# Kernel optimization log

Hardware: AMD Instinct MI355X
Metric: run time of the kernel (lower is better)

## Reference

```python
import jax, jax.numpy as jnp
import numpy as np

B, S, D, H = 2, 2048, 64, 12  # batch, seq, richness (per-head dim), heads
NEG = -99999.0


def setup_inputs() -> dict:
    key = jax.random.key(0)
    ks = jax.random.split(key, 9)
    s_in = 1.0 / np.sqrt(D)
    s_out = 1.0 / np.sqrt(H * D)
    return {
        "x": jax.random.normal(ks[0], (B, S, D), dtype=jnp.float32),
        "Wq": jax.random.uniform(ks[1], (D, H * D), jnp.float32, -s_in, s_in),
        "bq": jax.random.uniform(ks[2], (H * D,), jnp.float32, -s_in, s_in),
        "Wk": jax.random.uniform(ks[3], (D, H * D), jnp.float32, -s_in, s_in),
        "bk": jax.random.uniform(ks[4], (H * D,), jnp.float32, -s_in, s_in),
        "Wv": jax.random.uniform(ks[5], (D, H * D), jnp.float32, -s_in, s_in),
        "bv": jax.random.uniform(ks[6], (H * D,), jnp.float32, -s_in, s_in),
        "Wo": jax.random.uniform(ks[7], (H * D, D), jnp.float32, -s_out, s_out),
        "bo": jax.random.uniform(ks[8], (D,), jnp.float32, -s_out, s_out),
    }


def reference(x, Wq, bq, Wk, bk, Wv, bv, Wo, bo):
    b, s, d = x.shape
    def split_heads(y):
        return y.reshape(b, s, H, d).transpose(0, 2, 1, 3)  # [B,H,S,D]
    q = split_heads(x @ Wq + bq)
    k = split_heads(x @ Wk + bk)
    v = split_heads(x @ Wv + bv)
    # NOTE: no 1/sqrt(d) scaling, faithful to original module.
    scores = jnp.einsum("bhqd,bhkd->bhqk", q, k)  # [B,H,S,S]
    # Faithful quirky mask: tril of the scores, then mask where it's zero.
    mask = jnp.tril(scores)
    scores = jnp.where(mask == 0, NEG, scores)
    p = jax.nn.softmax(scores, axis=-1)
    o = jnp.einsum("bhqk,bhkd->bhqd", p, v)  # [B,H,S,D]
    o = o.transpose(0, 2, 1, 3).reshape(b, s, H * d)
    return o @ Wo + bo
```

## Files before the change

### kernel.cpp

```cpp
#include <hip/hip_runtime.h>
#include <math.h>
#include <type_traits>

#define BB 2
#define SS 2048
#define DD 64
#define HH 12
#define C2FIX 23.083120654223414f

typedef _Float16 v8h __attribute__((ext_vector_type(8)));
typedef short    v8s __attribute__((ext_vector_type(8)));
typedef short    v4s __attribute__((ext_vector_type(4)));
typedef float    v4f __attribute__((ext_vector_type(4)));
typedef unsigned int v2u __attribute__((ext_vector_type(2)));

__device__ __forceinline__ unsigned short f2bf(float f) {
    unsigned u = __float_as_uint(f);
    u += 0x7FFF + ((u >> 16) & 1);
    return (unsigned short)(u >> 16);
}

__device__ __forceinline__ void async16(const void* g, void* l) {
    __builtin_amdgcn_global_load_lds(
        (const __attribute__((address_space(1))) unsigned int*)g,
        (__attribute__((address_space(3))) unsigned int*)l, 16, 0, 0);
}

__global__ __launch_bounds__(256) void prep_kernel(
    const float* __restrict__ x,
    const float* __restrict__ Wq, const float* __restrict__ Wk,
    const float* __restrict__ Wv, const float* __restrict__ Wo,
    _Float16* __restrict__ x16, _Float16* __restrict__ W16,
    _Float16* __restrict__ WoT)
{
    const int idx = blockIdx.x * 256 + threadIdx.x;
    if (idx < 262144) {
        x16[idx] = (_Float16)x[idx];
    } else if (idx < 262144 + 147456) {
        const int t = idx - 262144;
        const int k = t / 2304, c = t % 2304;
        const int mat = c / 768, cc = c % 768;
        const float* W = (mat == 0) ? Wq : (mat == 1) ? Wk : Wv;
        W16[c * 64 + k] = (_Float16)W[k * 768 + cc];
    } else {
        const int e = idx - 262144 - 147456;
        WoT[(e & 63) * 768 + (e >> 6)] = (_Float16)Wo[e];
    }
}

__global__ __launch_bounds__(256) void qkv_kernel(
    const _Float16* __restrict__ x16, const _Float16* __restrict__ W16,
    const float* __restrict__ bq, const float* __restrict__ bk,
    const float* __restrict__ bv,
    _Float16* __restrict__ Q16, _Float16* __restrict__ K16,
    unsigned short* __restrict__ VT)
{
    const int r0  = blockIdx.x * 64;
    const int c0g = blockIdx.y * 64;
    const int mat = c0g / 768, cc0 = c0g % 768;
    const int h   = cc0 >> 6;
    const int b   = r0 >> 11, s0 = r0 & 2047;

    const int wave = threadIdx.x >> 6, lane = threadIdx.x & 63;
    const int llow = lane & 15, quad = lane >> 4;
    const int rowbase = r0 + 16 * wave;

    const float* bias = (mat == 0) ? bq : (mat == 1) ? bk : bv;

    v8h a0 = *(const v8h*)(x16 + (size_t)(rowbase + llow) * 64 + quad * 8);
    v8h a1 = *(const v8h*)(x16 + (size_t)(rowbase + llow) * 64 + 32 + quad * 8);

    v4f acc[4];
    float bv4[4];
#pragma unroll
    for (int nb = 0; nb < 4; nb++) {
        const int col = c0g + 16 * nb + llow;
        v8h b0 = *(const v8h*)(W16 + (size_t)col * 64 + quad * 8);
        v8h b1 = *(const v8h*)(W16 + (size_t)col * 64 + 32 + quad * 8);
        v4f a = (v4f){0.f, 0.f, 0.f, 0.f};
        a = __builtin_amdgcn_mfma_f32_16x16x32_f16(a0, b0, a, 0, 0, 0);
        a = __builtin_amdgcn_mfma_f32_16x16x32_f16(a1, b1, a, 0, 0, 0);
        acc[nb] = a;
        bv4[nb] = bias[cc0 + 16 * nb + llow];
    }

    const int bh = b * HH + h;
    if (mat == 0) {
#pragma unroll
        for (int nb = 0; nb < 4; nb++)
#pragma unroll
            for (int r = 0; r < 4; r++) {
                const int s = s0 + 16 * wave + quad * 4 + r;
                Q16[((size_t)bh * SS + s) * 64 + 16 * nb + llow] =
                    (_Float16)((acc[nb][r] + bv4[nb]) * 1.4426950408889634f);
            }
    } else if (mat == 1) {
#pragma unroll
        for (int nb = 0; nb < 4; nb++)
#pragma unroll
            for (int r = 0; r < 4; r++) {
                const int s = s0 + 16 * wave + quad * 4 + r;
                K16[((size_t)bh * SS + s) * 64 + 16 * nb + llow] =
                    (_Float16)(acc[nb][r] + bv4[nb]);
            }
    } else {
#pragma unroll
        for (int nb = 0; nb < 4; nb++) {
            const int d = 16 * nb + llow;
            const int s = s0 + 16 * wave + quad * 4;
            unsigned short p0 = f2bf(acc[nb][0] + bv4[nb]);
            unsigned short p1 = f2bf(acc[nb][1] + bv4[nb]);
            unsigned short p2 = f2bf(acc[nb][2] + bv4[nb]);
            unsigned short p3 = f2bf(acc[nb][3] + bv4[nb]);
            v2u pk = (v2u){(unsigned)p0 | ((unsigned)p1 << 16),
                           (unsigned)p2 | ((unsigned)p3 << 16)};
            *(v2u*)&VT[((size_t)bh * 64 + d) * SS + s] = pk;
        }
    }
}

__global__ __launch_bounds__(256, 4) void attn_kernel(
    const _Float16* __restrict__ Q16, const _Float16* __restrict__ K16,
    const unsigned short* __restrict__ VTg, _Float16* __restrict__ O16)
{
    __shared__ __align__(16) _Float16       Kl[2][64 * 64];
    __shared__ __align__(16) unsigned short Vl[2][64 * 64];

    const int bh    = blockIdx.y;
    const int qtile = (int)((blockIdx.x + 11 * blockIdx.y) & 31);
    const int qBase = qtile * 64;
    const int wave  = threadIdx.x >> 6;
    const int lane  = threadIdx.x & 63;
    const int llow  = lane & 15;
    const int quad  = lane >> 4;
    const int q0    = qBase + 16 * wave;

    const _Float16*       Kp = K16 + (size_t)bh * SS * 64;
    const unsigned short* Vp = VTg + (size_t)bh * 64 * SS;

    const _Float16* Qp = Q16 + ((size_t)bh * SS + q0) * 64;
    v8h qa0 = *(const v8h*)(Qp + llow * 64 + quad * 8);
    v8h qa1 = *(const v8h*)(Qp + llow * 64 + 32 + quad * 8);

    v4f o[4];
    v4f ls = (v4f){0.f, 0.f, 0.f, 0.f};
    const short one_bf = (short)0x3F80;
    const v4s vones = (v4s){one_bf, one_bf, one_bf, one_bf};
#pragma unroll
    for (int nb = 0; nb < 4; nb++) o[nb] = (v4f){0.f, 0.f, 0.f, 0.f};

    const int nt = qtile + 1;
    const int qrow = q0 + llow;
    const int sw = llow & 7;

#pragma unroll
    for (int rep = 0; rep < 2; rep++) {
        int c = rep * 256 + threadIdx.x;
        int row = c >> 3, g = (c & 7) ^ (row & 7);
        async16(Kp + (size_t)row * 64 + g * 8, &Kl[0][(rep * 256 + wave * 64) * 8]);
        async16(Vp + (size_t)row * SS + g * 8, &Vl[0][(rep * 256 + wave * 64) * 8]);
    }

    auto tile_body = [&](int t, auto masked_c) {
        constexpr bool MASKED = decltype(masked_c)::value;
        __syncthreads();
        if (t + 1 < nt) {
            const int ktn = (t + 1) * 64, bufn = (t + 1) & 1;
#pragma unroll
            for (int rep = 0; rep < 2; rep++) {
                int c = rep * 256 + threadIdx.x;
                int row = c >> 3, g = (c & 7) ^ (row & 7);
                async16(Kp + (size_t)(ktn + row) * 64 + g * 8,
                        &Kl[bufn][(rep * 256 + wave * 64) * 8]);
                async16(Vp + (size_t)row * SS + ktn + g * 8,
                        &Vl[bufn][(rep * 256 + wave * 64) * 8]);
            }
        }
        const int buf = t & 1, kt = t * 64;

        v4f sc[4];
#pragma unroll
        for (int cb = 0; cb < 4; cb++) {
            const int rk = 16 * cb + llow;
            v8h k0 = *(const v8h*)&Kl[buf][rk * 64 + ((quad ^ sw)) * 8];
            v8h k1 = *(const v8h*)&Kl[buf][rk * 64 + (((4 + quad) ^ sw)) * 8];
            v4f a2 = (v4f){0.f, 0.f, 0.f, 0.f};
            a2 = __builtin_amdgcn_mfma_f32_16x16x32_f16(k0, qa0, a2, 0, 0, 0);
            a2 = __builtin_amdgcn_mfma_f32_16x16x32_f16(k1, qa1, a2, 0, 0, 0);
            sc[cb] = a2;
        }

        v4s vvf[4][4];
#pragma unroll
        for (int nb = 0; nb < 4; nb++) {
            const int rv = 16 * nb + llow;
#pragma unroll
            for (int cb = 0; cb < 4; cb++)
                vvf[nb][cb] = *(const v4s*)&Vl[buf][rv * 64 +
                                (((2 * cb + (quad >> 1)) ^ sw) * 8) + (quad & 1) * 4];
        }

        v4s pA[4];
#pragma unroll
        for (int cb = 0; cb < 4; cb++) {
            const int kbase = kt + 16 * cb + quad * 4;
            unsigned dw[2];
#pragma unroll
            for (int h2 = 0; h2 < 2; h2++) {
                float pv2[2];
#pragma unroll
                for (int j2 = 0; j2 < 2; j2++) {
                    const int r = h2 * 2 + j2;
                    const float sv = sc[cb][r];
                    const float e  = __builtin_amdgcn_exp2f(sv - C2FIX);
                    float p;
                    if constexpr (MASKED)
                        p = (kbase + r <= qrow && sv != 0.f) ? e : 0.f;
                    else
                        p = (sv != 0.f) ? e : 0.f;
                    pv2[j2] = p;
                }
                dw[h2] = __builtin_amdgcn_perm(__float_as_uint(pv2[1]),
                                               __float_as_uint(pv2[0]),
                                               0x07060302u);
            }
            v2u pk = (v2u){dw[0], dw[1]};
            pA[cb] = *(const v4s*)&pk;
        }

#pragma unroll
        for (int cb = 0; cb < 4; cb++)
            ls = __builtin_amdgcn_mfma_f32_16x16x16bf16_1k(pA[cb], vones, ls, 0, 0, 0);

#pragma unroll
        for (int nb = 0; nb < 4; nb++)
#pragma unroll
            for (int cb = 0; cb < 4; cb++)
                o[nb] = __builtin_amdgcn_mfma_f32_16x16x16bf16_1k(
                            pA[cb], vvf[nb][cb], o[nb], 0, 0, 0);
    };

    for (int t = 0; t < nt - 1; t++) tile_body(t, std::false_type{});
    tile_body(nt - 1, std::true_type{});

    float ir[4];
#pragma unroll
    for (int r = 0; r < 4; r++)
        ir[r] = 1.0f / ls[r];
    _Float16* Op = O16 + ((size_t)bh * SS + q0) * 64;
#pragma unroll
    for (int nb = 0; nb < 4; nb++)
#pragma unroll
        for (int r = 0; r < 4; r++)
            Op[(quad * 4 + r) * 64 + 16 * nb + llow] = (_Float16)(o[nb][r] * ir[r]);
}

__global__ __launch_bounds__(256) void out_kernel(
    const _Float16* __restrict__ O16, const _Float16* __restrict__ WoT,
    const float* __restrict__ bo, float* __restrict__ out)
{
    __shared__ __align__(16) float red[4][16][66];
    const int r0   = blockIdx.x * 16;
    const int wave = threadIdx.x >> 6, lane = threadIdx.x & 63;
    const int llow = lane & 15, quad = lane >> 4;
    const int b = r0 >> 11, s = r0 & 2047;

    v4f acc[4];
#pragma unroll
    for (int cb = 0; cb < 4; cb++) acc[cb] = (v4f){0.f, 0.f, 0.f, 0.f};

#pragma unroll
    for (int i = 0; i < 6; i++) {
        const int kb = wave * 6 + i;
        const int h = kb >> 1, dseg = (kb & 1) * 32;
        v8h af = *(const v8h*)(O16 + ((size_t)(b * HH + h) * SS + s + llow) * 64 + dseg + quad * 8);
#pragma unroll
        for (int cb = 0; cb < 4; cb++) {
            v8h bf = *(const v8h*)(WoT + (size_t)(16 * cb + llow) * 768 + kb * 32 + quad * 8);
            acc[cb] = __builtin_amdgcn_mfma_f32_16x16x32_f16(af, bf, acc[cb], 0, 0, 0);
        }
    }

#pragma unroll
    for (int cb = 0; cb < 4; cb++)
#pragma unroll
        for (int r = 0; r < 4; r++)
            red[wave][quad * 4 + r][16 * cb + llow] = acc[cb][r];
    __syncthreads();

    const int col = threadIdx.x & 63, rr = threadIdx.x >> 6;
    const float bias = bo[col];
    for (int i = rr; i < 16; i += 4) {
        float sum = red[0][i][col] + red[1][i][col] + red[2][i][col] + red[3][i][col] + bias;
        out[(size_t)(r0 + i) * 64 + col] = sum;
    }
}

extern "C" void kernel_launch(void* const* d_in, const int* in_sizes, int n_in,
                              void* d_out, int out_size, void* d_ws, size_t ws_size,
                              hipStream_t stream)
{
    const float* x  = (const float*)d_in[0];
    const float* Wq = (const float*)d_in[1];
    const float* bq = (const float*)d_in[2];
    const float* Wk = (const float*)d_in[3];
    const float* bk = (const float*)d_in[4];
    const float* Wv = (const float*)d_in[5];
    const float* bv = (const float*)d_in[6];
    const float* Wo = (const float*)d_in[7];
    const float* bo = (const float*)d_in[8];
    float* out = (float*)d_out;

    char* w = (char*)d_ws;
    const size_t MB = 1024 * 1024;
    _Float16*       x16 = (_Float16*)(w);
    _Float16*       W16 = (_Float16*)(w + 512 * 1024);
    _Float16*       WoT = (_Float16*)(w + 832 * 1024);
    _Float16*       Q16 = (_Float16*)(w + 1 * MB);
    _Float16*       K16 = (_Float16*)(w + 7 * MB);
    unsigned short* VT  = (unsigned short*)(w + 13 * MB);
    _Float16*       O16 = (_Float16*)(w + 19 * MB);

    prep_kernel<<<1792, 256, 0, stream>>>(x, Wq, Wk, Wv, Wo, x16, W16, WoT);
    qkv_kernel<<<dim3(64, 36), 256, 0, stream>>>(x16, W16, bq, bk, bv, Q16, K16, VT);
    attn_kernel<<<dim3(32, BB * HH), 256, 0, stream>>>(Q16, K16, VT, O16);
    out_kernel<<<(BB * SS) / 16, 256, 0, stream>>>(O16, WoT, bo, out);
}
```

Baseline: 135.7 us.

## Triple-buffer K/V tiles with explicit vmcnt waits for deeper prefetch

```diff
diff --git a/kernel.cpp b/kernel.cpp
--- a/kernel.cpp
+++ b/kernel.cpp
@@ -119,12 +119,12 @@
     }
 }
 
-__global__ __launch_bounds__(256, 4) void attn_kernel(
+__global__ __launch_bounds__(256, 3) void attn_kernel(
     const _Float16* __restrict__ Q16, const _Float16* __restrict__ K16,
     const unsigned short* __restrict__ VTg, _Float16* __restrict__ O16)
 {
-    __shared__ __align__(16) _Float16       Kl[2][64 * 64];
-    __shared__ __align__(16) unsigned short Vl[2][64 * 64];
+    __shared__ __align__(16) _Float16       Kl[3][64 * 64];
+    __shared__ __align__(16) unsigned short Vl[3][64 * 64];
 
     const int bh    = blockIdx.y;
     const int qtile = (int)((blockIdx.x + 11 * blockIdx.y) & 31);
@@ -153,30 +153,31 @@
     const int qrow = q0 + llow;
     const int sw = llow & 7;
 
-#pragma unroll
-    for (int rep = 0; rep < 2; rep++) {
-        int c = rep * 256 + threadIdx.x;
-        int row = c >> 3, g = (c & 7) ^ (row & 7);
-        async16(Kp + (size_t)row * 64 + g * 8, &Kl[0][(rep * 256 + wave * 64) * 8]);
-        async16(Vp + (size_t)row * SS + g * 8, &Vl[0][(rep * 256 + wave * 64) * 8]);
-    }
-
-    auto tile_body = [&](int t, auto masked_c) {
+    auto stage = [&](int kt, int b) {
+#pragma unroll
+        for (int rep = 0; rep < 2; rep++) {
+            int c = rep * 256 + threadIdx.x;
+            int row = c >> 3, g = (c & 7) ^ (row & 7);
+            async16(Kp + (size_t)(kt + row) * 64 + g * 8,
+                    &Kl[b][(rep * 256 + wave * 64) * 8]);
+            async16(Vp + (size_t)row * SS + kt + g * 8,
+                    &Vl[b][(rep * 256 + wave * 64) * 8]);
+        }
+    };
+
+    stage(0, 0);
+    if (nt > 1) stage(64, 1);
+
+    auto round_body = [&](int t, auto masked_c) {
         constexpr bool MASKED = decltype(masked_c)::value;
-        __syncthreads();
-        if (t + 1 < nt) {
-            const int ktn = (t + 1) * 64, bufn = (t + 1) & 1;
-#pragma unroll
-            for (int rep = 0; rep < 2; rep++) {
-                int c = rep * 256 + threadIdx.x;
-                int row = c >> 3, g = (c & 7) ^ (row & 7);
-                async16(Kp + (size_t)(ktn + row) * 64 + g * 8,
-                        &Kl[bufn][(rep * 256 + wave * 64) * 8]);
-                async16(Vp + (size_t)row * SS + ktn + g * 8,
-                        &Vl[bufn][(rep * 256 + wave * 64) * 8]);
-            }
-        }
-        const int buf = t & 1, kt = t * 64;
+        if constexpr (MASKED)
+            asm volatile("s_waitcnt vmcnt(0)" ::: "memory");
+        else
+            asm volatile("s_waitcnt vmcnt(4)" ::: "memory");
+        __builtin_amdgcn_s_barrier();
+        __builtin_amdgcn_sched_barrier(0);
+        if (t + 2 < nt) stage((t + 2) * 64, (t + 2) % 3);
+        const int buf = t % 3, kt = t * 64;
 
         v4f sc[4];
 #pragma unroll
@@ -240,8 +241,8 @@
                             pA[cb], vvf[nb][cb], o[nb], 0, 0, 0);
     };
 
-    for (int t = 0; t < nt - 1; t++) tile_body(t, std::false_type{});
-    tile_body(nt - 1, std::true_type{});
+    for (int t = 0; t < nt - 1; t++) round_body(t, std::false_type{});
+    round_body(nt - 1, std::true_type{});
 
     float ir[4];
 #pragma unroll
```

After: 133.4 us. No clear change (-1.7%).
